# Kernel tuning notes

Measured on AMD Instinct MI355X. Metric: run time of the kernel, lower is better.

## Reference

```python
import jax, jax.numpy as jnp
import numpy as np
from jax import lax

KSIZE = 11
SIGMA = 1.5
C1 = (0.01 * 1.0) ** 2
C2 = (0.03 * 1.0) ** 2
PAD = (KSIZE - 1) // 2  # 5


def _gaussian_2d(ksize: int, sigma: float) -> np.ndarray:
    half = (ksize - 1) * 0.5
    g = np.exp(-0.5 * (np.linspace(-half, half, ksize) / sigma) ** 2)
    g = g / g.sum()
    return np.outer(g, g).astype(np.float32)  # [k, k]


def setup_inputs() -> dict:
    key = jax.random.key(0)
    kx, ky = jax.random.split(key)
    B, C, T, H, W = 2, 3, 8, 512, 512
    x = jax.random.uniform(kx, (B, C, T, H, W), dtype=jnp.float32)
    y = jax.random.uniform(ky, (B, C, T, H, W), dtype=jnp.float32)
    k2d = jnp.asarray(_gaussian_2d(KSIZE, SIGMA))
    # depthwise conv3d kernel: [C_out=C, C_in/groups=1, kD=1, kH, kW]
    kernel = jnp.broadcast_to(k2d[None, None, None], (C, 1, 1, KSIZE, KSIZE))
    return {"x": x, "y": y, "kernel": kernel}


def reference(x, y, kernel):
    C = x.shape[1]

    def conv(z):
        return lax.conv_general_dilated(
            z, kernel,
            window_strides=(1, 1, 1),
            padding=((0, 0), (PAD, PAD), (PAD, PAD)),
            dimension_numbers=("NCDHW", "OIDHW", "NCDHW"),
            feature_group_count=C,
        )

    # single grouped conv over the 5 stacked statistics, as in the original
    stacked = jnp.concatenate([x, y, x * x, y * y, x * y], axis=0)
    ux, uy, uxx, uyy, uxy = jnp.split(conv(stacked), 5, axis=0)

    vx = uxx - ux * ux
    vy = uyy - uy * uy
    vxy = uxy - ux * uy
    a1 = 2.0 * ux * uy + C1
    a2 = 2.0 * vxy + C2
    b1 = ux * ux + uy * uy + C1
    b2 = vx + vy + C2
    return a1 * a2 / (b1 * b2)
```

## Files before the change

kernel.cpp:

```cpp
#include <hip/hip_runtime.h>
#include <type_traits>

namespace {
constexpr int HH = 512;
constexpr int WW = 512;
constexpr int KS = 11;
constexpr int PADR = 5;
constexpr int TH = 32;
constexpr int TW = 64;
constexpr int SLAB = 16;
constexpr int HC = TW + 2 * PADR;
constexpr int LPA = 148;
constexpr int LPC = 76;
constexpr int NTHREADS = 256;
constexpr float SSIM_C1 = 1.0e-4f;
constexpr float SSIM_C2 = 9.0e-4f;
}

typedef float v2f __attribute__((ext_vector_type(2)));
typedef float v4f __attribute__((ext_vector_type(4)));
#define LOWP(v)  __builtin_shufflevector(v, v, 0, 1)
#define HIGHP(v) __builtin_shufflevector(v, v, 2, 3)

__global__ __launch_bounds__(NTHREADS, 6) void ssim_fused(
    const float* __restrict__ x, const float* __restrict__ y,
    const float* __restrict__ kern, float* __restrict__ out)
{
    __shared__ __align__(16) float pA[SLAB][LPA];
    __shared__ __align__(16) float pB_[SLAB][LPA];
    __shared__ __align__(16) float pC_[SLAB][LPC];

    constexpr int tiles_w = WW / TW;
    constexpr int tiles_h = HH / TH;
    constexpr int tpp = tiles_w * tiles_h;

    const int bid = blockIdx.x;
    const int plane = bid / tpp;
    const int trem = bid - plane * tpp;
    const int tr_idx = trem / tiles_w;
    const int tile_r = tr_idx * TH;
    const int tile_c = (trem - tr_idx * tiles_w) * TW;

    const float* __restrict__ xp = x + (size_t)plane * (HH * WW);
    const float* __restrict__ yp = y + (size_t)plane * (HH * WW);
    float* __restrict__ op = out + (size_t)plane * (HH * WW);

    v2f pw[6];
    {
        const float inv = rsqrtf(kern[5 * KS + 5]);
#pragma unroll
        for (int i = 0; i < 6; ++i) {
            const float w = kern[5 * KS + i] * inv;
            v2f tmp = {w, w};
            pw[i] = tmp;
        }
    }

    const int t = threadIdx.x;
    const bool interior = (tile_r >= PADR) && (tile_r + TH + PADR <= HH) &&
                          (tile_c >= PADR) && (tile_c + TW + PADR <= WW);

    const int p2_r = t >> 4;
    const int p2_m = t & 15;

    auto run_slab = [&](int s0, auto intr_tag) {
        constexpr bool INTR = decltype(intr_tag)::value;
        for (int i = t; i < (SLAB / 2) * HC; i += NTHREADS) {
            const int r2 = i / HC;
            const int c = i - r2 * HC;
            const int gr = tile_r + s0 + 2 * r2;
            const int gc = tile_c + c - PADR;
            v2f uvA = {0.f, 0.f}, qqA = {0.f, 0.f};
            v2f uvB = {0.f, 0.f}, qqB = {0.f, 0.f};
            float xyA = 0.f, xyB = 0.f;
            const float* xq = xp + (gr - PADR) * WW + gc;
            const float* yq = yp + (gr - PADR) * WW + gc;
#pragma unroll
            for (int k = 0; k < KS + 1; ++k) {
                float xv, yv;
                if (INTR) {
                    xv = xq[k * WW];
                    yv = yq[k * WW];
                } else {
                    const int rr = gr - PADR + k;
                    const bool ok = (gc >= 0) & (gc < WW) & (rr >= 0) & (rr < HH);
                    xv = 0.f; yv = 0.f;
                    if (ok) {
                        xv = xp[rr * WW + gc];
                        yv = yp[rr * WW + gc];
                    }
                }
                v2f v2 = {xv, yv};
                const v2f q2 = v2 * v2;
                const float xy = xv * yv;
                if (k < KS) {
                    const v2f w = pw[k < 6 ? k : 10 - k];
                    uvA += w * v2;
                    qqA += w * q2;
                    xyA += w.x * xy;
                }
                if (k >= 1) {
                    const v2f w = pw[(k - 1) < 6 ? (k - 1) : 11 - k];
                    uvB += w * v2;
                    qqB += w * q2;
                    xyB += w.x * xy;
                }
            }
            const int rA = 2 * r2, rB = 2 * r2 + 1;
            *(v2f*)&pA[rA][2 * c] = uvA;   *(v2f*)&pA[rB][2 * c] = uvB;
            *(v2f*)&pB_[rA][2 * c] = qqA;  *(v2f*)&pB_[rB][2 * c] = qqB;
            pC_[rA][c] = xyA;              pC_[rB][c] = xyB;
        }
        __syncthreads();

#define PCONV(R0, R1, R2, R3, a0, a1, a2, a3, a4, a5, a6)                       \
    R0 += pw[0]*LOWP(a0); R0 += pw[1]*HIGHP(a0); R0 += pw[2]*LOWP(a1);          \
    R0 += pw[3]*HIGHP(a1); R0 += pw[4]*LOWP(a2); R0 += pw[5]*HIGHP(a2);         \
    R0 += pw[4]*LOWP(a3); R0 += pw[3]*HIGHP(a3); R0 += pw[2]*LOWP(a4);          \
    R0 += pw[1]*HIGHP(a4); R0 += pw[0]*LOWP(a5);                                \
    R1 += pw[0]*HIGHP(a0); R1 += pw[1]*LOWP(a1); R1 += pw[2]*HIGHP(a1);         \
    R1 += pw[3]*LOWP(a2); R1 += pw[4]*HIGHP(a2); R1 += pw[5]*LOWP(a3);          \
    R1 += pw[4]*HIGHP(a3); R1 += pw[3]*LOWP(a4); R1 += pw[2]*HIGHP(a4);         \
    R1 += pw[1]*LOWP(a5); R1 += pw[0]*HIGHP(a5);                                \
    R2 += pw[0]*LOWP(a1); R2 += pw[1]*HIGHP(a1); R2 += pw[2]*LOWP(a2);          \
    R2 += pw[3]*HIGHP(a2); R2 += pw[4]*LOWP(a3); R2 += pw[5]*HIGHP(a3);         \
    R2 += pw[4]*LOWP(a4); R2 += pw[3]*HIGHP(a4); R2 += pw[2]*LOWP(a5);          \
    R2 += pw[1]*HIGHP(a5); R2 += pw[0]*LOWP(a6);                                \
    R3 += pw[0]*HIGHP(a1); R3 += pw[1]*LOWP(a2); R3 += pw[2]*HIGHP(a2);         \
    R3 += pw[3]*LOWP(a3); R3 += pw[4]*HIGHP(a3); R3 += pw[5]*LOWP(a4);          \
    R3 += pw[4]*HIGHP(a4); R3 += pw[3]*LOWP(a5); R3 += pw[2]*HIGHP(a5);         \
    R3 += pw[1]*LOWP(a6); R3 += pw[0]*HIGHP(a6);

#define SCONV(R, S0, S1, S2, S3, S4, S5, S6, S7, S8, S9, S10)                   \
    R += pw[0].x*S0; R += pw[1].x*S1; R += pw[2].x*S2; R += pw[3].x*S3;         \
    R += pw[4].x*S4; R += pw[5].x*S5; R += pw[4].x*S6; R += pw[3].x*S7;         \
    R += pw[2].x*S8; R += pw[1].x*S9; R += pw[0].x*S10;

        v2f rUV0 = {0.f, 0.f}, rUV1 = {0.f, 0.f}, rUV2 = {0.f, 0.f}, rUV3 = {0.f, 0.f};
        {
            const float* rowA = &pA[p2_r][8 * p2_m];
            const v4f a0 = *(const v4f*)(rowA + 0);
            const v4f a1 = *(const v4f*)(rowA + 4);
            const v4f a2 = *(const v4f*)(rowA + 8);
            const v4f a3 = *(const v4f*)(rowA + 12);
            const v4f a4 = *(const v4f*)(rowA + 16);
            const v4f a5 = *(const v4f*)(rowA + 20);
            const v4f a6 = *(const v4f*)(rowA + 24);
            PCONV(rUV0, rUV1, rUV2, rUV3, a0, a1, a2, a3, a4, a5, a6)
        }
        v2f rQQ0 = {0.f, 0.f}, rQQ1 = {0.f, 0.f}, rQQ2 = {0.f, 0.f}, rQQ3 = {0.f, 0.f};
        {
            const float* rowB = &pB_[p2_r][8 * p2_m];
            const v4f a0 = *(const v4f*)(rowB + 0);
            const v4f a1 = *(const v4f*)(rowB + 4);
            const v4f a2 = *(const v4f*)(rowB + 8);
            const v4f a3 = *(const v4f*)(rowB + 12);
            const v4f a4 = *(const v4f*)(rowB + 16);
            const v4f a5 = *(const v4f*)(rowB + 20);
            const v4f a6 = *(const v4f*)(rowB + 24);
            PCONV(rQQ0, rQQ1, rQQ2, rQQ3, a0, a1, a2, a3, a4, a5, a6)
        }
        float rC0 = 0.f, rC1 = 0.f, rC2 = 0.f, rC3 = 0.f;
        {
            const float* rowC = &pC_[p2_r][4 * p2_m];
            const v4f c0 = *(const v4f*)(rowC + 0);
            const v4f c1 = *(const v4f*)(rowC + 4);
            const v4f c2 = *(const v4f*)(rowC + 8);
            const v4f c3 = *(const v4f*)(rowC + 12);
            const float e0 = c0.x, e1 = c0.y, e2 = c0.z, e3 = c0.w;
            const float e4 = c1.x, e5 = c1.y, e6 = c1.z, e7 = c1.w;
            const float e8 = c2.x, e9 = c2.y, e10 = c2.z, e11 = c2.w;
            const float e12 = c3.x, e13 = c3.y;
            SCONV(rC0, e0, e1, e2, e3, e4, e5, e6, e7, e8, e9, e10)
            SCONV(rC1, e1, e2, e3, e4, e5, e6, e7, e8, e9, e10, e11)
            SCONV(rC2, e2, e3, e4, e5, e6, e7, e8, e9, e10, e11, e12)
            SCONV(rC3, e3, e4, e5, e6, e7, e8, e9, e10, e11, e12, e13)
        }

        float4 o4;
#pragma unroll
        for (int j = 0; j < 4; ++j) {
            const v2f uvj = (j == 0) ? rUV0 : (j == 1) ? rUV1 : (j == 2) ? rUV2 : rUV3;
            const v2f qqj = (j == 0) ? rQQ0 : (j == 1) ? rQQ1 : (j == 2) ? rQQ2 : rQQ3;
            const float uxy = (j == 0) ? rC0 : (j == 1) ? rC1 : (j == 2) ? rC2 : rC3;
            const float ux = uvj.x, uy = uvj.y;
            const float uxx = qqj.x, uyy = qqj.y;
            const float vx  = uxx - ux * ux;
            const float vy  = uyy - uy * uy;
            const float vxy = uxy - ux * uy;
            const float a1s = 2.f * ux * uy + SSIM_C1;
            const float a2s = 2.f * vxy + SSIM_C2;
            const float b1s = ux * ux + uy * uy + SSIM_C1;
            const float b2s = vx + vy + SSIM_C2;
            (&o4.x)[j] = (a1s * a2s) * __builtin_amdgcn_rcpf(b1s * b2s);
        }
        *(float4*)(op + (size_t)(tile_r + s0 + p2_r) * WW + (tile_c + 4 * p2_m)) = o4;
        __syncthreads();
#undef PCONV
#undef SCONV
    };

    if (interior) {
        run_slab(0,    std::true_type{});
        run_slab(SLAB, std::true_type{});
    } else {
        run_slab(0,    std::false_type{});
        run_slab(SLAB, std::false_type{});
    }
}

extern "C" void kernel_launch(void* const* d_in, const int* in_sizes, int n_in,
                              void* d_out, int out_size, void* d_ws, size_t ws_size,
                              hipStream_t stream) {
    const float* x    = (const float*)d_in[0];
    const float* y    = (const float*)d_in[1];
    const float* kern = (const float*)d_in[2];
    float* out = (float*)d_out;

    const int nplanes = in_sizes[0] / (HH * WW);
    const int nblocks = nplanes * (HH / TH) * (WW / TW);

    ssim_fused<<<dim3(nblocks), dim3(NTHREADS), 0, stream>>>(x, y, kern, out);
}
```

Baseline: 203.4 us.

## Give each wavefront a private LDS region to replace block barriers with wave syncs

Each of the four wavefronts now owns a private LDS slice and handles 8 output rows in two rounds of 4. This lets the block-wide __syncthreads be replaced by an LDS waitcnt and a wave barrier. The intent is to remove inter-wave barrier stalls so waves can overlap independently. The loop trip structure changes (2*HC items over 64 lanes), and the correctness of the intra-wave LDS ordering relies on lgkmcnt waits and the wave barrier.

After: 213.2 us. 4.8% more time.

```diff
diff --git a/kernel.cpp b/kernel.cpp
--- a/kernel.cpp
+++ b/kernel.cpp
@@ -8,11 +8,11 @@
 constexpr int PADR = 5;
 constexpr int TH = 32;
 constexpr int TW = 64;
-constexpr int SLAB = 16;
 constexpr int HC = TW + 2 * PADR;
 constexpr int LPA = 148;
 constexpr int LPC = 76;
 constexpr int NTHREADS = 256;
+constexpr int RROWS = 4;
 constexpr float SSIM_C1 = 1.0e-4f;
 constexpr float SSIM_C2 = 9.0e-4f;
 }
@@ -26,9 +26,9 @@
     const float* __restrict__ x, const float* __restrict__ y,
     const float* __restrict__ kern, float* __restrict__ out)
 {
-    __shared__ __align__(16) float pA[SLAB][LPA];
-    __shared__ __align__(16) float pB_[SLAB][LPA];
-    __shared__ __align__(16) float pC_[SLAB][LPC];
+    __shared__ __align__(16) float pA[4][RROWS * LPA];
+    __shared__ __align__(16) float pB_[4][RROWS * LPA];
+    __shared__ __align__(16) float pC_[4][RROWS * LPC];
 
     constexpr int tiles_w = WW / TW;
     constexpr int tiles_h = HH / TH;
@@ -57,18 +57,24 @@
     }
 
     const int t = threadIdx.x;
+    const int wv = t >> 6;
+    const int lane = t & 63;
     const bool interior = (tile_r >= PADR) && (tile_r + TH + PADR <= HH) &&
                           (tile_c >= PADR) && (tile_c + TW + PADR <= WW);
 
-    const int p2_r = t >> 4;
-    const int p2_m = t & 15;
-
-    auto run_slab = [&](int s0, auto intr_tag) {
+    float* const wA = pA[wv];
+    float* const wB = pB_[wv];
+    float* const wC = pC_[wv];
+
+    const int p2_r = lane >> 4;
+    const int p2_m = lane & 15;
+
+    auto run_round = [&](int base_r, auto intr_tag) {
         constexpr bool INTR = decltype(intr_tag)::value;
-        for (int i = t; i < (SLAB / 2) * HC; i += NTHREADS) {
-            const int r2 = i / HC;
+        for (int i = lane; i < 2 * HC; i += 64) {
+            const int r2 = (i >= HC) ? 1 : 0;
             const int c = i - r2 * HC;
-            const int gr = tile_r + s0 + 2 * r2;
+            const int gr = base_r + 2 * r2;
             const int gc = tile_c + c - PADR;
             v2f uvA = {0.f, 0.f}, qqA = {0.f, 0.f};
             v2f uvB = {0.f, 0.f}, qqB = {0.f, 0.f};
@@ -107,11 +113,11 @@
                 }
             }
             const int rA = 2 * r2, rB = 2 * r2 + 1;
-            *(v2f*)&pA[rA][2 * c] = uvA;   *(v2f*)&pA[rB][2 * c] = uvB;
-            *(v2f*)&pB_[rA][2 * c] = qqA;  *(v2f*)&pB_[rB][2 * c] = qqB;
-            pC_[rA][c] = xyA;              pC_[rB][c] = xyB;
-        }
-        __syncthreads();
+            *(v2f*)&wA[rA * LPA + 2 * c] = uvA;  *(v2f*)&wA[rB * LPA + 2 * c] = uvB;
+            *(v2f*)&wB[rA * LPA + 2 * c] = qqA;  *(v2f*)&wB[rB * LPA + 2 * c] = qqB;
+            wC[rA * LPC + c] = xyA;              wC[rB * LPC + c] = xyB;
+        }
+        asm volatile("s_waitcnt lgkmcnt(0)" ::: "memory");
 
 #define PCONV(R0, R1, R2, R3, a0, a1, a2, a3, a4, a5, a6)                       \
     R0 += pw[0]*LOWP(a0); R0 += pw[1]*HIGHP(a0); R0 += pw[2]*LOWP(a1);          \
@@ -138,7 +144,7 @@
 
         v2f rUV0 = {0.f, 0.f}, rUV1 = {0.f, 0.f}, rUV2 = {0.f, 0.f}, rUV3 = {0.f, 0.f};
         {
-            const float* rowA = &pA[p2_r][8 * p2_m];
+            const float* rowA = &wA[p2_r * LPA + 8 * p2_m];
             const v4f a0 = *(const v4f*)(rowA + 0);
             const v4f a1 = *(const v4f*)(rowA + 4);
             const v4f a2 = *(const v4f*)(rowA + 8);
@@ -150,7 +156,7 @@
         }
         v2f rQQ0 = {0.f, 0.f}, rQQ1 = {0.f, 0.f}, rQQ2 = {0.f, 0.f}, rQQ3 = {0.f, 0.f};
         {
-            const float* rowB = &pB_[p2_r][8 * p2_m];
+            const float* rowB = &wB[p2_r * LPA + 8 * p2_m];
             const v4f a0 = *(const v4f*)(rowB + 0);
             const v4f a1 = *(const v4f*)(rowB + 4);
             const v4f a2 = *(const v4f*)(rowB + 8);
@@ -162,7 +168,7 @@
         }
         float rC0 = 0.f, rC1 = 0.f, rC2 = 0.f, rC3 = 0.f;
         {
-            const float* rowC = &pC_[p2_r][4 * p2_m];
+            const float* rowC = &wC[p2_r * LPC + 4 * p2_m];
             const v4f c0 = *(const v4f*)(rowC + 0);
             const v4f c1 = *(const v4f*)(rowC + 4);
             const v4f c2 = *(const v4f*)(rowC + 8);
@@ -194,18 +200,19 @@
             const float b2s = vx + vy + SSIM_C2;
             (&o4.x)[j] = (a1s * a2s) * __builtin_amdgcn_rcpf(b1s * b2s);
         }
-        *(float4*)(op + (size_t)(tile_r + s0 + p2_r) * WW + (tile_c + 4 * p2_m)) = o4;
-        __syncthreads();
+        *(float4*)(op + (size_t)(base_r + p2_r) * WW + (tile_c + 4 * p2_m)) = o4;
+        __builtin_amdgcn_wave_barrier();
 #undef PCONV
 #undef SCONV
     };
 
+    const int wrow = tile_r + 8 * wv;
     if (interior) {
-        run_slab(0,    std::true_type{});
-        run_slab(SLAB, std::true_type{});
+        run_round(wrow,         std::true_type{});
+        run_round(wrow + RROWS, std::true_type{});
     } else {
-        run_slab(0,    std::false_type{});
-        run_slab(SLAB, std::false_type{});
+        run_round(wrow,         std::false_type{});
+        run_round(wrow + RROWS, std::false_type{});
     }
 }
 
```

## Process column pairs with 8-byte loads and halve block size to 128 threads

Applied to the files above, without the earlier changes.

The vertical pass now has each thread handle two adjacent columns, using 8-byte vector loads of x and y. The column window shifts to start at tile_c-6 so the pair loads stay aligned, and shared-memory offsets are adjusted to match. The block drops to 128 threads with 8-row slabs, run four times per tile, which aims to cut per-thread load instructions and shared memory per block so more blocks fit per CU. The cost is more barriers per tile and wider per-thread register state, and the launch_bounds hint was not updated for the new thread count.

Measured after the change: 273.6 us. 34.5% more time.

```diff
diff --git a/kernel.cpp b/kernel.cpp
--- a/kernel.cpp
+++ b/kernel.cpp
@@ -8,11 +8,11 @@
 constexpr int PADR = 5;
 constexpr int TH = 32;
 constexpr int TW = 64;
-constexpr int SLAB = 16;
-constexpr int HC = TW + 2 * PADR;
-constexpr int LPA = 148;
-constexpr int LPC = 76;
-constexpr int NTHREADS = 256;
+constexpr int SLAB = 8;
+constexpr int NCP = 38;
+constexpr int PAF = 180;
+constexpr int PCF = 84;
+constexpr int NTHREADS = 128;
 constexpr float SSIM_C1 = 1.0e-4f;
 constexpr float SSIM_C2 = 9.0e-4f;
 }
@@ -26,9 +26,9 @@
     const float* __restrict__ x, const float* __restrict__ y,
     const float* __restrict__ kern, float* __restrict__ out)
 {
-    __shared__ __align__(16) float pA[SLAB][LPA];
-    __shared__ __align__(16) float pB_[SLAB][LPA];
-    __shared__ __align__(16) float pC_[SLAB][LPC];
+    __shared__ __align__(16) float pA[SLAB * PAF];
+    __shared__ __align__(16) float pB_[SLAB * PAF];
+    __shared__ __align__(16) float pC_[SLAB * PCF];
 
     constexpr int tiles_w = WW / TW;
     constexpr int tiles_h = HH / TH;
@@ -58,78 +58,86 @@
 
     const int t = threadIdx.x;
     const bool interior = (tile_r >= PADR) && (tile_r + TH + PADR <= HH) &&
-                          (tile_c >= PADR) && (tile_c + TW + PADR <= WW);
+                          (tile_c >= 6) && (tile_c + 70 <= WW);
 
     const int p2_r = t >> 4;
     const int p2_m = t & 15;
 
     auto run_slab = [&](int s0, auto intr_tag) {
         constexpr bool INTR = decltype(intr_tag)::value;
-        for (int i = t; i < (SLAB / 2) * HC; i += NTHREADS) {
-            const int r2 = i / HC;
-            const int c = i - r2 * HC;
+        for (int i = t; i < 4 * NCP; i += NTHREADS) {
+            const int r2 = i / NCP;
+            const int cp = i - r2 * NCP;
             const int gr = tile_r + s0 + 2 * r2;
-            const int gc = tile_c + c - PADR;
-            v2f uvA = {0.f, 0.f}, qqA = {0.f, 0.f};
-            v2f uvB = {0.f, 0.f}, qqB = {0.f, 0.f};
-            float xyA = 0.f, xyB = 0.f;
+            const int gc = tile_c - 6 + 2 * cp;
+            v2f sxA = {0.f, 0.f}, syA = {0.f, 0.f}, sxxA = {0.f, 0.f},
+                syyA = {0.f, 0.f}, sxyA = {0.f, 0.f};
+            v2f sxB = {0.f, 0.f}, syB = {0.f, 0.f}, sxxB = {0.f, 0.f},
+                syyB = {0.f, 0.f}, sxyB = {0.f, 0.f};
             const float* xq = xp + (gr - PADR) * WW + gc;
             const float* yq = yp + (gr - PADR) * WW + gc;
 #pragma unroll
             for (int k = 0; k < KS + 1; ++k) {
-                float xv, yv;
+                v2f xv, yv;
                 if (INTR) {
-                    xv = xq[k * WW];
-                    yv = yq[k * WW];
+                    xv = *(const v2f*)(xq + k * WW);
+                    yv = *(const v2f*)(yq + k * WW);
                 } else {
                     const int rr = gr - PADR + k;
-                    const bool ok = (gc >= 0) & (gc < WW) & (rr >= 0) & (rr < HH);
-                    xv = 0.f; yv = 0.f;
-                    if (ok) {
-                        xv = xp[rr * WW + gc];
-                        yv = yp[rr * WW + gc];
+                    const bool okr = (rr >= 0) & (rr < HH);
+                    float x0 = 0.f, x1 = 0.f, y0 = 0.f, y1 = 0.f;
+                    if (okr & (gc >= 0) & (gc < WW)) {
+                        x0 = xp[rr * WW + gc];
+                        y0 = yp[rr * WW + gc];
                     }
+                    if (okr & (gc + 1 >= 0) & (gc + 1 < WW)) {
+                        x1 = xp[rr * WW + gc + 1];
+                        y1 = yp[rr * WW + gc + 1];
+                    }
+                    v2f tx = {x0, x1}; xv = tx;
+                    v2f ty = {y0, y1}; yv = ty;
                 }
-                v2f v2 = {xv, yv};
-                const v2f q2 = v2 * v2;
-                const float xy = xv * yv;
+                const v2f xx = xv * xv;
+                const v2f yy = yv * yv;
+                const v2f xy = xv * yv;
                 if (k < KS) {
                     const v2f w = pw[k < 6 ? k : 10 - k];
-                    uvA += w * v2;
-                    qqA += w * q2;
-                    xyA += w.x * xy;
+                    sxA += w * xv;  syA += w * yv;
+                    sxxA += w * xx; syyA += w * yy; sxyA += w * xy;
                 }
                 if (k >= 1) {
                     const v2f w = pw[(k - 1) < 6 ? (k - 1) : 11 - k];
-                    uvB += w * v2;
-                    qqB += w * q2;
-                    xyB += w.x * xy;
+                    sxB += w * xv;  syB += w * yv;
+                    sxxB += w * xx; syyB += w * yy; sxyB += w * xy;
                 }
             }
             const int rA = 2 * r2, rB = 2 * r2 + 1;
-            *(v2f*)&pA[rA][2 * c] = uvA;   *(v2f*)&pA[rB][2 * c] = uvB;
-            *(v2f*)&pB_[rA][2 * c] = qqA;  *(v2f*)&pB_[rB][2 * c] = qqB;
-            pC_[rA][c] = xyA;              pC_[rB][c] = xyB;
+            v4f uA = {sxA.x, syA.x, sxA.y, syA.y};
+            v4f qA = {sxxA.x, syyA.x, sxxA.y, syyA.y};
+            v4f uB = {sxB.x, syB.x, sxB.y, syB.y};
+            v4f qB = {sxxB.x, syyB.x, sxxB.y, syyB.y};
+            *(v4f*)&pA[rA * PAF + 4 * cp] = uA;
+            *(v4f*)&pA[rB * PAF + 4 * cp] = uB;
+            *(v4f*)&pB_[rA * PAF + 4 * cp] = qA;
+            *(v4f*)&pB_[rB * PAF + 4 * cp] = qB;
+            *(v2f*)&pC_[rA * PCF + 2 * cp] = sxyA;
+            *(v2f*)&pC_[rB * PCF + 2 * cp] = sxyB;
         }
         __syncthreads();
 
-#define PCONV(R0, R1, R2, R3, a0, a1, a2, a3, a4, a5, a6)                       \
-    R0 += pw[0]*LOWP(a0); R0 += pw[1]*HIGHP(a0); R0 += pw[2]*LOWP(a1);          \
-    R0 += pw[3]*HIGHP(a1); R0 += pw[4]*LOWP(a2); R0 += pw[5]*HIGHP(a2);         \
-    R0 += pw[4]*LOWP(a3); R0 += pw[3]*HIGHP(a3); R0 += pw[2]*LOWP(a4);          \
-    R0 += pw[1]*HIGHP(a4); R0 += pw[0]*LOWP(a5);                                \
-    R1 += pw[0]*HIGHP(a0); R1 += pw[1]*LOWP(a1); R1 += pw[2]*HIGHP(a1);         \
-    R1 += pw[3]*LOWP(a2); R1 += pw[4]*HIGHP(a2); R1 += pw[5]*LOWP(a3);          \
-    R1 += pw[4]*HIGHP(a3); R1 += pw[3]*LOWP(a4); R1 += pw[2]*HIGHP(a4);         \
-    R1 += pw[1]*LOWP(a5); R1 += pw[0]*HIGHP(a5);                                \
-    R2 += pw[0]*LOWP(a1); R2 += pw[1]*HIGHP(a1); R2 += pw[2]*LOWP(a2);          \
-    R2 += pw[3]*HIGHP(a2); R2 += pw[4]*LOWP(a3); R2 += pw[5]*HIGHP(a3);         \
-    R2 += pw[4]*LOWP(a4); R2 += pw[3]*HIGHP(a4); R2 += pw[2]*LOWP(a5);          \
-    R2 += pw[1]*HIGHP(a5); R2 += pw[0]*LOWP(a6);                                \
-    R3 += pw[0]*HIGHP(a1); R3 += pw[1]*LOWP(a2); R3 += pw[2]*HIGHP(a2);         \
-    R3 += pw[3]*LOWP(a3); R3 += pw[4]*HIGHP(a3); R3 += pw[5]*LOWP(a4);          \
-    R3 += pw[4]*HIGHP(a4); R3 += pw[3]*LOWP(a5); R3 += pw[2]*HIGHP(a5);         \
-    R3 += pw[1]*LOWP(a6); R3 += pw[0]*HIGHP(a6);
+#define PCONV(R0, R1, R2, R3, P0, P1, P2, P3, P4, P5, P6, P7, P8, P9, P10, P11, P12, P13) \
+    R0 += pw[0]*P0; R0 += pw[1]*P1; R0 += pw[2]*P2; R0 += pw[3]*P3;             \
+    R0 += pw[4]*P4; R0 += pw[5]*P5; R0 += pw[4]*P6; R0 += pw[3]*P7;             \
+    R0 += pw[2]*P8; R0 += pw[1]*P9; R0 += pw[0]*P10;                            \
+    R1 += pw[0]*P1; R1 += pw[1]*P2; R1 += pw[2]*P3; R1 += pw[3]*P4;             \
+    R1 += pw[4]*P5; R1 += pw[5]*P6; R1 += pw[4]*P7; R1 += pw[3]*P8;             \
+    R1 += pw[2]*P9; R1 += pw[1]*P10; R1 += pw[0]*P11;                           \
+    R2 += pw[0]*P2; R2 += pw[1]*P3; R2 += pw[2]*P4; R2 += pw[3]*P5;             \
+    R2 += pw[4]*P6; R2 += pw[5]*P7; R2 += pw[4]*P8; R2 += pw[3]*P9;             \
+    R2 += pw[2]*P10; R2 += pw[1]*P11; R2 += pw[0]*P12;                          \
+    R3 += pw[0]*P3; R3 += pw[1]*P4; R3 += pw[2]*P5; R3 += pw[3]*P6;             \
+    R3 += pw[4]*P7; R3 += pw[5]*P8; R3 += pw[4]*P9; R3 += pw[3]*P10;            \
+    R3 += pw[2]*P11; R3 += pw[1]*P12; R3 += pw[0]*P13;
 
 #define SCONV(R, S0, S1, S2, S3, S4, S5, S6, S7, S8, S9, S10)                   \
     R += pw[0].x*S0; R += pw[1].x*S1; R += pw[2].x*S2; R += pw[3].x*S3;         \
@@ -138,43 +146,51 @@
 
         v2f rUV0 = {0.f, 0.f}, rUV1 = {0.f, 0.f}, rUV2 = {0.f, 0.f}, rUV3 = {0.f, 0.f};
         {
-            const float* rowA = &pA[p2_r][8 * p2_m];
-            const v4f a0 = *(const v4f*)(rowA + 0);
-            const v4f a1 = *(const v4f*)(rowA + 4);
-            const v4f a2 = *(const v4f*)(rowA + 8);
-            const v4f a3 = *(const v4f*)(rowA + 12);
-            const v4f a4 = *(const v4f*)(rowA + 16);
-            const v4f a5 = *(const v4f*)(rowA + 20);
-            const v4f a6 = *(const v4f*)(rowA + 24);
-            PCONV(rUV0, rUV1, rUV2, rUV3, a0, a1, a2, a3, a4, a5, a6)
+            const float* rowA = &pA[p2_r * PAF + 8 * p2_m];
+            const v4f b0 = *(const v4f*)(rowA + 0);
+            const v4f b1 = *(const v4f*)(rowA + 4);
+            const v4f b2 = *(const v4f*)(rowA + 8);
+            const v4f b3 = *(const v4f*)(rowA + 12);
+            const v4f b4 = *(const v4f*)(rowA + 16);
+            const v4f b5 = *(const v4f*)(rowA + 20);
+            const v4f b6 = *(const v4f*)(rowA + 24);
+            const v4f b7 = *(const v4f*)(rowA + 28);
+            PCONV(rUV0, rUV1, rUV2, rUV3,
+                  HIGHP(b0), LOWP(b1), HIGHP(b1), LOWP(b2), HIGHP(b2),
+                  LOWP(b3), HIGHP(b3), LOWP(b4), HIGHP(b4), LOWP(b5),
+                  HIGHP(b5), LOWP(b6), HIGHP(b6), LOWP(b7))
         }
         v2f rQQ0 = {0.f, 0.f}, rQQ1 = {0.f, 0.f}, rQQ2 = {0.f, 0.f}, rQQ3 = {0.f, 0.f};
         {
-            const float* rowB = &pB_[p2_r][8 * p2_m];
-            const v4f a0 = *(const v4f*)(rowB + 0);
-            const v4f a1 = *(const v4f*)(rowB + 4);
-            const v4f a2 = *(const v4f*)(rowB + 8);
-            const v4f a3 = *(const v4f*)(rowB + 12);
-            const v4f a4 = *(const v4f*)(rowB + 16);
-            const v4f a5 = *(const v4f*)(rowB + 20);
-            const v4f a6 = *(const v4f*)(rowB + 24);
-            PCONV(rQQ0, rQQ1, rQQ2, rQQ3, a0, a1, a2, a3, a4, a5, a6)
+            const float* rowB = &pB_[p2_r * PAF + 8 * p2_m];
+            const v4f b0 = *(const v4f*)(rowB + 0);
+            const v4f b1 = *(const v4f*)(rowB + 4);
+            const v4f b2 = *(const v4f*)(rowB + 8);
+            const v4f b3 = *(const v4f*)(rowB + 12);
+            const v4f b4 = *(const v4f*)(rowB + 16);
+            const v4f b5 = *(const v4f*)(rowB + 20);
+            const v4f b6 = *(const v4f*)(rowB + 24);
+            const v4f b7 = *(const v4f*)(rowB + 28);
+            PCONV(rQQ0, rQQ1, rQQ2, rQQ3,
+                  HIGHP(b0), LOWP(b1), HIGHP(b1), LOWP(b2), HIGHP(b2),
+                  LOWP(b3), HIGHP(b3), LOWP(b4), HIGHP(b4), LOWP(b5),
+                  HIGHP(b5), LOWP(b6), HIGHP(b6), LOWP(b7))
         }
         float rC0 = 0.f, rC1 = 0.f, rC2 = 0.f, rC3 = 0.f;
         {
-            const float* rowC = &pC_[p2_r][4 * p2_m];
+            const float* rowC = &pC_[p2_r * PCF + 4 * p2_m];
             const v4f c0 = *(const v4f*)(rowC + 0);
             const v4f c1 = *(const v4f*)(rowC + 4);
             const v4f c2 = *(const v4f*)(rowC + 8);
             const v4f c3 = *(const v4f*)(rowC + 12);
-            const float e0 = c0.x, e1 = c0.y, e2 = c0.z, e3 = c0.w;
-            const float e4 = c1.x, e5 = c1.y, e6 = c1.z, e7 = c1.w;
-            const float e8 = c2.x, e9 = c2.y, e10 = c2.z, e11 = c2.w;
-            const float e12 = c3.x, e13 = c3.y;
-            SCONV(rC0, e0, e1, e2, e3, e4, e5, e6, e7, e8, e9, e10)
-            SCONV(rC1, e1, e2, e3, e4, e5, e6, e7, e8, e9, e10, e11)
-            SCONV(rC2, e2, e3, e4, e5, e6, e7, e8, e9, e10, e11, e12)
-            SCONV(rC3, e3, e4, e5, e6, e7, e8, e9, e10, e11, e12, e13)
+            const float f1 = c0.y, f2 = c0.z, f3 = c0.w;
+            const float f4 = c1.x, f5 = c1.y, f6 = c1.z, f7 = c1.w;
+            const float f8 = c2.x, f9 = c2.y, f10 = c2.z, f11 = c2.w;
+            const float f12 = c3.x, f13 = c3.y, f14 = c3.z;
+            SCONV(rC0, f1, f2, f3, f4, f5, f6, f7, f8, f9, f10, f11)
+            SCONV(rC1, f2, f3, f4, f5, f6, f7, f8, f9, f10, f11, f12)
+            SCONV(rC2, f3, f4, f5, f6, f7, f8, f9, f10, f11, f12, f13)
+            SCONV(rC3, f4, f5, f6, f7, f8, f9, f10, f11, f12, f13, f14)
         }
 
         float4 o4;
@@ -201,11 +217,15 @@
     };
 
     if (interior) {
-        run_slab(0,    std::true_type{});
-        run_slab(SLAB, std::true_type{});
+        run_slab(0,         std::true_type{});
+        run_slab(SLAB,      std::true_type{});
+        run_slab(2 * SLAB,  std::true_type{});
+        run_slab(3 * SLAB,  std::true_type{});
     } else {
-        run_slab(0,    std::false_type{});
-        run_slab(SLAB, std::false_type{});
+        run_slab(0,         std::false_type{});
+        run_slab(SLAB,      std::false_type{});
+        run_slab(2 * SLAB,  std::false_type{});
+        run_slab(3 * SLAB,  std::false_type{});
     }
 }
 
```
